# Kernel tuning notes

Measured on AMD Instinct MI355X. Metric: run time of the kernel, lower is better.

The kernel has to match this reference:

```python
import jax, jax.numpy as jnp
import numpy as np

N = 8192
D_IN = 128
D_OUT = 128


def setup_inputs() -> dict:
    key = jax.random.key(0)
    k1, k2, k3 = jax.random.split(key, 3)
    x = jax.random.normal(k1, (N, D_IN), dtype=jnp.float32)
    adj = jax.random.uniform(k2, (N, N), dtype=jnp.float32)  # dense adjacency / edge weights
    weight = jax.random.normal(k3, (D_IN, D_OUT), dtype=jnp.float32) * (1.0 / np.sqrt(D_IN))
    bias = jnp.zeros((D_OUT,), dtype=jnp.float32)
    return {"x": x, "adj": adj, "weight": weight, "bias": bias}


def gcn_norm(adj, add_self_loops=False):
    # symmetric normalization: D^{-1/2} A D^{-1/2}
    if add_self_loops:
        adj = adj + jnp.eye(adj.shape[0], dtype=adj.dtype)
    deg = adj.sum(axis=1)
    dinv = jnp.where(deg > 0, jax.lax.rsqrt(deg), 0.0)  # masked_fill(isinf, 0)
    return adj * dinv[:, None] * dinv[None, :]


def reference(x, adj, weight, bias):
    adj_n = gcn_norm(adj, add_self_loops=False)  # cached normalized adjacency
    h = x @ weight                               # [N, D_out] dense projection
    out = adj_n @ h + bias                       # neighborhood aggregation + bias
    return out
```

## Files before the change

kernel.cpp:

```cpp
#include <hip/hip_runtime.h>
#include <hip/hip_bf16.h>

#define NN 8192
#define DD 128

typedef __attribute__((ext_vector_type(4))) float f32x4;
typedef __attribute__((ext_vector_type(8))) short s16x8;
typedef __attribute__((ext_vector_type(4))) short s16x4;

__device__ inline short bfbits(float f) {
    unsigned u = __builtin_bit_cast(unsigned, f);
    u += 0x7fffu + ((u >> 16) & 1u);
    return (short)(u >> 16);
}

__device__ inline s16x4 cvt4(f32x4 a) {
    s16x4 r;
    r[0] = bfbits(a[0]); r[1] = bfbits(a[1]); r[2] = bfbits(a[2]); r[3] = bfbits(a[3]);
    return r;
}

__device__ inline s16x8 cvt8(f32x4 a, f32x4 b) {
    s16x8 r;
    r[0] = bfbits(a[0]); r[1] = bfbits(a[1]); r[2] = bfbits(a[2]); r[3] = bfbits(a[3]);
    r[4] = bfbits(b[0]); r[5] = bfbits(b[1]); r[6] = bfbits(b[2]); r[7] = bfbits(b[3]);
    return r;
}

__global__ __launch_bounds__(256) void deg_kernel(const float* __restrict__ adj,
                                                  float* __restrict__ dinv) {
    const int lane = threadIdx.x & 63;
    const int row  = (blockIdx.x << 2) + (threadIdx.x >> 6);
    const float* r = adj + (size_t)row * NN;

    f32x4 s0 = {0.f, 0.f, 0.f, 0.f};
    f32x4 s1 = {0.f, 0.f, 0.f, 0.f};
    #pragma unroll 8
    for (int it = 0; it < 32; it += 2) {
        f32x4 v0 = *(const f32x4*)(r + it * 256 + (lane << 2));
        f32x4 v1 = *(const f32x4*)(r + (it + 1) * 256 + (lane << 2));
        s0 += v0;
        s1 += v1;
    }
    f32x4 s = s0 + s1;
    float sum = s[0] + s[1] + s[2] + s[3];
    #pragma unroll
    for (int off = 32; off; off >>= 1) sum += __shfl_xor(sum, off, 64);
    if (lane == 0) dinv[row] = (sum > 0.f) ? rsqrtf(sum) : 0.f;
}

#define WST 132
__global__ __launch_bounds__(256) void proj_kernel(const float* __restrict__ x,
                                                   const float* __restrict__ w,
                                                   const float* __restrict__ dinv,
                                                   unsigned short* __restrict__ h2f) {
    __shared__ short lds_w[128 * WST];
    const int tid  = threadIdx.x;
    const int lane = tid & 63;
    const int wave = tid >> 6;
    const int j0   = blockIdx.x << 4;
    const int n0   = wave << 5;
    const int r    = lane & 15;
    const int q    = lane >> 4;

    #pragma unroll
    for (int i = 0; i < 16; ++i) {
        int gi = i * 256 + tid;
        int k  = gi >> 5;
        int n4 = (gi & 31) << 2;
        f32x4 v = *(const f32x4*)(w + (size_t)k * DD + n4);
        *(s16x4*)&lds_w[k * WST + n4] = cvt4(v);
    }
    __syncthreads();

    const float* xp = x + (size_t)(j0 + r) * DD + (q << 3);

    f32x4 acc0 = {0.f, 0.f, 0.f, 0.f};
    f32x4 acc1 = {0.f, 0.f, 0.f, 0.f};

    #pragma unroll
    for (int k = 0; k < DD; k += 32) {
        f32x4 a0 = *(const f32x4*)(xp + k);
        f32x4 a1 = *(const f32x4*)(xp + k + 4);
        s16x8 af = cvt8(a0, a1);

        const int kb = k + (q << 3);
        s16x8 b0, b1;
        #pragma unroll
        for (int jj = 0; jj < 8; ++jj) {
            b0[jj] = lds_w[(kb + jj) * WST + n0 + r];
            b1[jj] = lds_w[(kb + jj) * WST + n0 + 16 + r];
        }
        acc0 = __builtin_amdgcn_mfma_f32_16x16x32_bf16(af, b0, acc0, 0, 0, 0);
        acc1 = __builtin_amdgcn_mfma_f32_16x16x32_bf16(af, b1, acc1, 0, 0, 0);
    }

    #pragma unroll
    for (int rr = 0; rr < 4; ++rr) {
        const int j = j0 + (q << 2) + rr;
        const float dv = dinv[j];
        const int kg = j >> 5, qp = (j >> 3) & 3, jj = j & 7;
        #pragma unroll
        for (int half = 0; half < 2; ++half) {
            const int n = n0 + half * 16 + r;
            const int f = n >> 4;
            const int lanep = qp * 16 + (n & 15);
            const float v = (half ? acc1[rr] : acc0[rr]) * dv;
            h2f[((((size_t)f << 8) + kg) << 6 | lanep) * 8 + jj] = (unsigned short)bfbits(v);
        }
    }
}

template <int KSPLIT>
__global__ __launch_bounds__(256, 8) void agg_kernel(const float* __restrict__ adj,
                                                     const unsigned short* __restrict__ h2f,
                                                     const float* __restrict__ dinv,
                                                     const float* __restrict__ bias,
                                                     float* __restrict__ dst) {
    constexpr int KS    = NN / KSPLIT;
    constexpr int TILES = KS / 128;
    __shared__ short lds_a[2][16 * 16 * 8];

    const int tid  = threadIdx.x;
    const int lane = tid & 63;
    const int wave = tid >> 6;
    const int r    = lane & 15;
    const int q    = lane >> 4;
    const int m0   = blockIdx.x << 4;
    const int k0   = blockIdx.y * KS;

    const int row0 = tid >> 5;
    const int off0 = (tid & 31) << 2;
    const int cd   = (tid & 31) >> 1;
    const int hh   = tid & 1;
    const int so0  = ((row0 << 4) + (cd ^ row0)) * 8 + hh * 4;
    const int so1  = (((8 + row0) << 4) + (cd ^ (8 + row0))) * 8 + hh * 4;

    const float* ap0 = adj + (size_t)(m0 + row0) * NN + k0 + off0;
    const float* ap1 = adj + (size_t)(m0 + 8 + row0) * NN + k0 + off0;

    const unsigned short* bb0 = h2f + (((size_t)(wave * 2)     * 256 + (k0 >> 5)) * 64 + lane) * 8;
    const unsigned short* bb1 = h2f + (((size_t)(wave * 2 + 1) * 256 + (k0 >> 5)) * 64 + lane) * 8;

    f32x4 acc0 = {0.f, 0.f, 0.f, 0.f};
    f32x4 acc1 = {0.f, 0.f, 0.f, 0.f};

    {
        f32x4 v0 = *(const f32x4*)(ap0);
        f32x4 v1 = *(const f32x4*)(ap1);
        *(s16x4*)&lds_a[0][so0] = cvt4(v0);
        *(s16x4*)&lds_a[0][so1] = cvt4(v1);
    }
    __syncthreads();

    for (int t = 0; t < TILES; ++t) {
        const short* lcur = lds_a[t & 1];
        short* lnxt = (short*)lds_a[(t + 1) & 1];

        s16x8 br0[4], br1[4];
        #pragma unroll
        for (int s = 0; s < 4; ++s) {
            br0[s] = *(const s16x8*)(bb0 + (size_t)(t * 4 + s) * 512);
            br1[s] = *(const s16x8*)(bb1 + (size_t)(t * 4 + s) * 512);
        }
        f32x4 v0, v1;
        if (t + 1 < TILES) {
            v0 = *(const f32x4*)(ap0 + (t + 1) * 128);
            v1 = *(const f32x4*)(ap1 + (t + 1) * 128);
        }
        #pragma unroll
        for (int s = 0; s < 4; ++s) {
            const int slot = (r << 4) + (((s << 2) + q) ^ r);
            s16x8 af = *(const s16x8*)(lcur + slot * 8);
            acc0 = __builtin_amdgcn_mfma_f32_16x16x32_bf16(af, br0[s], acc0, 0, 0, 0);
            acc1 = __builtin_amdgcn_mfma_f32_16x16x32_bf16(af, br1[s], acc1, 0, 0, 0);
        }
        if (t + 1 < TILES) {
            *(s16x4*)(lnxt + so0) = cvt4(v0);
            *(s16x4*)(lnxt + so1) = cvt4(v1);
        }
        __syncthreads();
    }

    #pragma unroll
    for (int rr = 0; rr < 4; ++rr) {
        const int m = m0 + (q << 2) + rr;
        const int n = (wave << 5) + r;
        if (KSPLIT == 1) {
            const float dv = dinv[m];
            dst[(size_t)m * DD + n]      = acc0[rr] * dv + bias[n];
            dst[(size_t)m * DD + n + 16] = acc1[rr] * dv + bias[n + 16];
        } else {
            float* p = dst + (size_t)blockIdx.y * NN * DD;
            p[(size_t)m * DD + n]      = acc0[rr];
            p[(size_t)m * DD + n + 16] = acc1[rr];
        }
    }
}

template <int KSPLIT>
__global__ __launch_bounds__(256) void reduce_kernel(const float* __restrict__ part,
                                                     const float* __restrict__ dinv,
                                                     const float* __restrict__ bias,
                                                     float* __restrict__ out) {
    const int idx = blockIdx.x * 256 + threadIdx.x;
    f32x4 s = ((const f32x4*)part)[idx];
    #pragma unroll
    for (int p = 1; p < KSPLIT; ++p)
        s += ((const f32x4*)part)[idx + (size_t)p * (NN * DD / 4)];
    const float dv = dinv[idx >> 5];
    const f32x4 bi = *(const f32x4*)(bias + ((idx & 31) << 2));
    f32x4 o;
    o[0] = s[0] * dv + bi[0]; o[1] = s[1] * dv + bi[1];
    o[2] = s[2] * dv + bi[2]; o[3] = s[3] * dv + bi[3];
    ((f32x4*)out)[idx] = o;
}

extern "C" void kernel_launch(void* const* d_in, const int* in_sizes, int n_in,
                              void* d_out, int out_size, void* d_ws, size_t ws_size,
                              hipStream_t stream) {
    const float* x    = (const float*)d_in[0];
    const float* adj  = (const float*)d_in[1];
    const float* w    = (const float*)d_in[2];
    const float* bias = (const float*)d_in[3];
    float* out = (float*)d_out;

    float* dinv = (float*)d_ws;
    unsigned short* h2f = (unsigned short*)((char*)d_ws + 32 * 1024);
    float* part = (float*)((char*)d_ws + 32 * 1024 + 2 * 1024 * 1024);
    const size_t need4 = 32 * 1024 + 2 * 1024 * 1024 + (size_t)4 * NN * DD * sizeof(float);
    const size_t need2 = 32 * 1024 + 2 * 1024 * 1024 + (size_t)2 * NN * DD * sizeof(float);

    deg_kernel<<<NN / 4, 256, 0, stream>>>(adj, dinv);
    proj_kernel<<<NN / 16, 256, 0, stream>>>(x, w, dinv, h2f);

    if (ws_size >= need4) {
        agg_kernel<4><<<dim3(NN / 16, 4), 256, 0, stream>>>(adj, h2f, dinv, bias, part);
        reduce_kernel<4><<<NN * DD / 4 / 256, 256, 0, stream>>>(part, dinv, bias, out);
    } else if (ws_size >= need2) {
        agg_kernel<2><<<dim3(NN / 16, 2), 256, 0, stream>>>(adj, h2f, dinv, bias, part);
        reduce_kernel<2><<<NN * DD / 4 / 256, 256, 0, stream>>>(part, dinv, bias, out);
    } else {
        agg_kernel<1><<<dim3(NN / 16, 1), 256, 0, stream>>>(adj, h2f, dinv, bias, out);
    }
}
```

Before: 444.7 us.

## Pre-convert adjacency to bf16 MFMA layout in degree pass, stream it in aggregation

```diff
diff --git a/kernel.cpp b/kernel.cpp
--- a/kernel.cpp
+++ b/kernel.cpp
@@ -7,6 +7,9 @@
 typedef __attribute__((ext_vector_type(4))) float f32x4;
 typedef __attribute__((ext_vector_type(8))) short s16x8;
 typedef __attribute__((ext_vector_type(4))) short s16x4;
+
+template <typename T>
+__device__ inline T ntload(const T* p) { return __builtin_nontemporal_load(p); }
 
 __device__ inline short bfbits(float f) {
     unsigned u = __builtin_bit_cast(unsigned, f);
@@ -28,25 +31,59 @@
 }
 
 __global__ __launch_bounds__(256) void deg_kernel(const float* __restrict__ adj,
-                                                  float* __restrict__ dinv) {
-    const int lane = threadIdx.x & 63;
-    const int row  = (blockIdx.x << 2) + (threadIdx.x >> 6);
-    const float* r = adj + (size_t)row * NN;
+                                                  float* __restrict__ dinv,
+                                                  unsigned short* __restrict__ abf) {
+    __shared__ short lds[2][2048];
+    const int t  = threadIdx.x;
+    const int m0 = blockIdx.x << 4;
+    const int r0 = t >> 5;
+    const int r1 = r0 + 8;
+    const int c  = (t & 31) << 2;
+    const int kgl = c >> 5;
+    const int q   = (c >> 3) & 3;
+    const int jj  = c & 7;
+    const int so0 = kgl * 512 + ((q << 4) + r0) * 8 + jj;
+    const int so1 = kgl * 512 + ((q << 4) + r1) * 8 + jj;
+
+    const float* ap0 = adj + (size_t)(m0 + r0) * NN + c;
+    const float* ap1 = adj + (size_t)(m0 + r1) * NN + c;
+    unsigned short* wp = abf + (((size_t)blockIdx.x * 256 + (t >> 6)) * 64 + (t & 63)) * 8;
 
     f32x4 s0 = {0.f, 0.f, 0.f, 0.f};
     f32x4 s1 = {0.f, 0.f, 0.f, 0.f};
-    #pragma unroll 8
-    for (int it = 0; it < 32; it += 2) {
-        f32x4 v0 = *(const f32x4*)(r + it * 256 + (lane << 2));
-        f32x4 v1 = *(const f32x4*)(r + (it + 1) * 256 + (lane << 2));
+
+    f32x4 v0 = ntload((const f32x4*)ap0);
+    f32x4 v1 = ntload((const f32x4*)ap1);
+
+    for (int ch = 0; ch < 64; ++ch) {
+        const int b = ch & 1;
         s0 += v0;
         s1 += v1;
-    }
-    f32x4 s = s0 + s1;
-    float sum = s[0] + s[1] + s[2] + s[3];
-    #pragma unroll
-    for (int off = 32; off; off >>= 1) sum += __shfl_xor(sum, off, 64);
-    if (lane == 0) dinv[row] = (sum > 0.f) ? rsqrtf(sum) : 0.f;
+        *(s16x4*)&lds[b][so0] = cvt4(v0);
+        *(s16x4*)&lds[b][so1] = cvt4(v1);
+        f32x4 n0, n1;
+        if (ch < 63) {
+            n0 = ntload((const f32x4*)(ap0 + (ch + 1) * 128));
+            n1 = ntload((const f32x4*)(ap1 + (ch + 1) * 128));
+        }
+        __syncthreads();
+        s16x8 wv = *(const s16x8*)&lds[b][t * 8];
+        *(s16x8*)(wp + (size_t)ch * 2048) = wv;
+        v0 = n0;
+        v1 = n1;
+    }
+
+    float a0 = s0[0] + s0[1] + s0[2] + s0[3];
+    float a1 = s1[0] + s1[1] + s1[2] + s1[3];
+    #pragma unroll
+    for (int off = 16; off; off >>= 1) {
+        a0 += __shfl_xor(a0, off, 64);
+        a1 += __shfl_xor(a1, off, 64);
+    }
+    if ((t & 31) == 0) {
+        dinv[m0 + r0] = (a0 > 0.f) ? rsqrtf(a0) : 0.f;
+        dinv[m0 + r1] = (a1 > 0.f) ? rsqrtf(a1) : 0.f;
+    }
 }
 
 #define WST 132
@@ -99,101 +136,73 @@
     for (int rr = 0; rr < 4; ++rr) {
         const int j = j0 + (q << 2) + rr;
         const float dv = dinv[j];
-        const int kg = j >> 5, qp = (j >> 3) & 3, jj = j & 7;
+        const int kg = j >> 5, qp = (j >> 3) & 3, jjj = j & 7;
         #pragma unroll
         for (int half = 0; half < 2; ++half) {
             const int n = n0 + half * 16 + r;
             const int f = n >> 4;
             const int lanep = qp * 16 + (n & 15);
             const float v = (half ? acc1[rr] : acc0[rr]) * dv;
-            h2f[((((size_t)f << 8) + kg) << 6 | lanep) * 8 + jj] = (unsigned short)bfbits(v);
+            h2f[(((size_t)f * 256 + kg) * 64 + lanep) * 8 + jjj] = (unsigned short)bfbits(v);
         }
     }
 }
 
 template <int KSPLIT>
-__global__ __launch_bounds__(256, 8) void agg_kernel(const float* __restrict__ adj,
+__global__ __launch_bounds__(256, 4) void agg_kernel(const unsigned short* __restrict__ abf,
                                                      const unsigned short* __restrict__ h2f,
                                                      const float* __restrict__ dinv,
                                                      const float* __restrict__ bias,
                                                      float* __restrict__ dst) {
-    constexpr int KS    = NN / KSPLIT;
-    constexpr int TILES = KS / 128;
-    __shared__ short lds_a[2][16 * 16 * 8];
-
-    const int tid  = threadIdx.x;
-    const int lane = tid & 63;
-    const int wave = tid >> 6;
+    constexpr int KGS = (NN / KSPLIT) >> 5;
+    const int lane = threadIdx.x & 63;
+    const int wave = threadIdx.x >> 6;
     const int r    = lane & 15;
     const int q    = lane >> 4;
-    const int m0   = blockIdx.x << 4;
-    const int k0   = blockIdx.y * KS;
-
-    const int row0 = tid >> 5;
-    const int off0 = (tid & 31) << 2;
-    const int cd   = (tid & 31) >> 1;
-    const int hh   = tid & 1;
-    const int so0  = ((row0 << 4) + (cd ^ row0)) * 8 + hh * 4;
-    const int so1  = (((8 + row0) << 4) + (cd ^ (8 + row0))) * 8 + hh * 4;
-
-    const float* ap0 = adj + (size_t)(m0 + row0) * NN + k0 + off0;
-    const float* ap1 = adj + (size_t)(m0 + 8 + row0) * NN + k0 + off0;
-
-    const unsigned short* bb0 = h2f + (((size_t)(wave * 2)     * 256 + (k0 >> 5)) * 64 + lane) * 8;
-    const unsigned short* bb1 = h2f + (((size_t)(wave * 2 + 1) * 256 + (k0 >> 5)) * 64 + lane) * 8;
-
-    f32x4 acc0 = {0.f, 0.f, 0.f, 0.f};
-    f32x4 acc1 = {0.f, 0.f, 0.f, 0.f};
-
-    {
-        f32x4 v0 = *(const f32x4*)(ap0);
-        f32x4 v1 = *(const f32x4*)(ap1);
-        *(s16x4*)&lds_a[0][so0] = cvt4(v0);
-        *(s16x4*)&lds_a[0][so1] = cvt4(v1);
-    }
-    __syncthreads();
-
-    for (int t = 0; t < TILES; ++t) {
-        const short* lcur = lds_a[t & 1];
-        short* lnxt = (short*)lds_a[(t + 1) & 1];
-
-        s16x8 br0[4], br1[4];
-        #pragma unroll
-        for (int s = 0; s < 4; ++s) {
-            br0[s] = *(const s16x8*)(bb0 + (size_t)(t * 4 + s) * 512);
-            br1[s] = *(const s16x8*)(bb1 + (size_t)(t * 4 + s) * 512);
-        }
-        f32x4 v0, v1;
-        if (t + 1 < TILES) {
-            v0 = *(const f32x4*)(ap0 + (t + 1) * 128);
-            v1 = *(const f32x4*)(ap1 + (t + 1) * 128);
-        }
-        #pragma unroll
-        for (int s = 0; s < 4; ++s) {
-            const int slot = (r << 4) + (((s << 2) + q) ^ r);
-            s16x8 af = *(const s16x8*)(lcur + slot * 8);
-            acc0 = __builtin_amdgcn_mfma_f32_16x16x32_bf16(af, br0[s], acc0, 0, 0, 0);
-            acc1 = __builtin_amdgcn_mfma_f32_16x16x32_bf16(af, br1[s], acc1, 0, 0, 0);
-        }
-        if (t + 1 < TILES) {
-            *(s16x4*)(lnxt + so0) = cvt4(v0);
-            *(s16x4*)(lnxt + so1) = cvt4(v1);
-        }
-        __syncthreads();
-    }
-
+    const int mt   = (int)(gridDim.x - 1 - blockIdx.x);
+    const int m0   = mt << 5;
+    const int kg0  = blockIdx.y * KGS;
+    const int f0   = wave << 1;
+
+    const unsigned short* a0 = abf + (((size_t)(mt * 2)     * 256 + kg0) * 64 + lane) * 8;
+    const unsigned short* a1 = abf + (((size_t)(mt * 2 + 1) * 256 + kg0) * 64 + lane) * 8;
+    const unsigned short* b0 = h2f + (((size_t)f0       * 256 + kg0) * 64 + lane) * 8;
+    const unsigned short* b1 = h2f + (((size_t)(f0 + 1) * 256 + kg0) * 64 + lane) * 8;
+
+    f32x4 acc00 = {0.f, 0.f, 0.f, 0.f};
+    f32x4 acc01 = {0.f, 0.f, 0.f, 0.f};
+    f32x4 acc10 = {0.f, 0.f, 0.f, 0.f};
+    f32x4 acc11 = {0.f, 0.f, 0.f, 0.f};
+
+    #pragma unroll 8
+    for (int kg = 0; kg < KGS; ++kg) {
+        s16x8 va0 = ntload((const s16x8*)(a0 + (size_t)kg * 512));
+        s16x8 va1 = ntload((const s16x8*)(a1 + (size_t)kg * 512));
+        s16x8 vb0 = *(const s16x8*)(b0 + (size_t)kg * 512);
+        s16x8 vb1 = *(const s16x8*)(b1 + (size_t)kg * 512);
+        acc00 = __builtin_amdgcn_mfma_f32_16x16x32_bf16(va0, vb0, acc00, 0, 0, 0);
+        acc01 = __builtin_amdgcn_mfma_f32_16x16x32_bf16(va0, vb1, acc01, 0, 0, 0);
+        acc10 = __builtin_amdgcn_mfma_f32_16x16x32_bf16(va1, vb0, acc10, 0, 0, 0);
+        acc11 = __builtin_amdgcn_mfma_f32_16x16x32_bf16(va1, vb1, acc11, 0, 0, 0);
+    }
+
+    const int n = (wave << 5) + r;
     #pragma unroll
     for (int rr = 0; rr < 4; ++rr) {
-        const int m = m0 + (q << 2) + rr;
-        const int n = (wave << 5) + r;
+        const int ma = m0 + (q << 2) + rr;
+        const int mb = ma + 16;
         if (KSPLIT == 1) {
-            const float dv = dinv[m];
-            dst[(size_t)m * DD + n]      = acc0[rr] * dv + bias[n];
-            dst[(size_t)m * DD + n + 16] = acc1[rr] * dv + bias[n + 16];
+            const float dva = dinv[ma], dvb = dinv[mb];
+            dst[(size_t)ma * DD + n]      = acc00[rr] * dva + bias[n];
+            dst[(size_t)ma * DD + n + 16] = acc01[rr] * dva + bias[n + 16];
+            dst[(size_t)mb * DD + n]      = acc10[rr] * dvb + bias[n];
+            dst[(size_t)mb * DD + n + 16] = acc11[rr] * dvb + bias[n + 16];
         } else {
             float* p = dst + (size_t)blockIdx.y * NN * DD;
-            p[(size_t)m * DD + n]      = acc0[rr];
-            p[(size_t)m * DD + n + 16] = acc1[rr];
+            p[(size_t)ma * DD + n]      = acc00[rr];
+            p[(size_t)ma * DD + n + 16] = acc01[rr];
+            p[(size_t)mb * DD + n]      = acc10[rr];
+            p[(size_t)mb * DD + n + 16] = acc11[rr];
         }
     }
 }
@@ -204,10 +213,10 @@
                                                      const float* __restrict__ bias,
                                                      float* __restrict__ out) {
     const int idx = blockIdx.x * 256 + threadIdx.x;
-    f32x4 s = ((const f32x4*)part)[idx];
+    f32x4 s = ntload((const f32x4*)part + idx);
     #pragma unroll
     for (int p = 1; p < KSPLIT; ++p)
-        s += ((const f32x4*)part)[idx + (size_t)p * (NN * DD / 4)];
+        s += ntload((const f32x4*)part + idx + (size_t)p * (NN * DD / 4));
     const float dv = dinv[idx >> 5];
     const f32x4 bi = *(const f32x4*)(bias + ((idx & 31) << 2));
     f32x4 o;
@@ -227,20 +236,20 @@
 
     float* dinv = (float*)d_ws;
     unsigned short* h2f = (unsigned short*)((char*)d_ws + 32 * 1024);
-    float* part = (float*)((char*)d_ws + 32 * 1024 + 2 * 1024 * 1024);
-    const size_t need4 = 32 * 1024 + 2 * 1024 * 1024 + (size_t)4 * NN * DD * sizeof(float);
-    const size_t need2 = 32 * 1024 + 2 * 1024 * 1024 + (size_t)2 * NN * DD * sizeof(float);
-
-    deg_kernel<<<NN / 4, 256, 0, stream>>>(adj, dinv);
+    unsigned short* abf = (unsigned short*)((char*)d_ws + 32 * 1024 + 2 * 1024 * 1024);
+    float* part = (float*)((char*)d_ws + 32 * 1024 + 2 * 1024 * 1024 + (size_t)NN * NN * 2);
+
+    const size_t base  = 32 * 1024 + 2 * 1024 * 1024 + (size_t)NN * NN * 2;
+    const size_t need4 = base + (size_t)4 * NN * DD * sizeof(float);
+    const size_t need1 = base;
+
+    deg_kernel<<<NN / 16, 256, 0, stream>>>(adj, dinv, abf);
     proj_kernel<<<NN / 16, 256, 0, stream>>>(x, w, dinv, h2f);
 
     if (ws_size >= need4) {
-        agg_kernel<4><<<dim3(NN / 16, 4), 256, 0, stream>>>(adj, h2f, dinv, bias, part);
+        agg_kernel<4><<<dim3(NN / 32, 4), 256, 0, stream>>>(abf, h2f, dinv, bias, part);
         reduce_kernel<4><<<NN * DD / 4 / 256, 256, 0, stream>>>(part, dinv, bias, out);
-    } else if (ws_size >= need2) {
-        agg_kernel<2><<<dim3(NN / 16, 2), 256, 0, stream>>>(adj, h2f, dinv, bias, part);
-        reduce_kernel<2><<<NN * DD / 4 / 256, 256, 0, stream>>>(part, dinv, bias, out);
-    } else {
-        agg_kernel<1><<<dim3(NN / 16, 1), 256, 0, stream>>>(adj, h2f, dinv, bias, out);
-    }
-}
+    } else if (ws_size >= need1) {
+        agg_kernel<1><<<dim3(NN / 32, 1), 256, 0, stream>>>(abf, h2f, dinv, bias, out);
+    }
+}
```

Result: slower. 459.5 us (+3.3%).
